# Performance work log

Measured on AMD Instinct MI355X. Metric: run time of the kernel, lower is better.

## Reference

```python
import jax, jax.numpy as jnp
import numpy as np
import math
from functools import partial

SIGMA0 = 12.0
KSIZE = int(2 * (4.0 * SIGMA0 + 0.5))  # 97, already odd
if KSIZE % 2 == 0:
    KSIZE -= 1


def _gauss1d(ksize, sigma):
    # kornia-style gaussian; ksize is odd so no half-pixel shift
    x = jnp.arange(ksize, dtype=jnp.float32) - ksize // 2
    g = jnp.exp(-(x ** 2) / (2.0 * sigma ** 2))
    return g / g.sum()


def _blur(x, sigma):
    # x: (N,1,H,W). filter2d with outer(kx,ky) kernel and constant(zero) border
    # == two separable 1D convs with zero 'SAME' padding.
    k = _gauss1d(KSIZE, sigma)
    dn = ('NCHW', 'OIHW', 'NCHW')
    x = jax.lax.conv_general_dilated(x, k[None, None, :, None], (1, 1), 'SAME', dimension_numbers=dn)
    x = jax.lax.conv_general_dilated(x, k[None, None, None, :], (1, 1), 'SAME', dimension_numbers=dn)
    return x


def _grid_sample_bilinear(img, grid):
    # img: (N,C,H,W); grid: (N,H,W,2) with last dim (x,y) in [-1,1], align_corners=True
    N, C, H, W = img.shape
    x = (grid[..., 0] + 1.0) * 0.5 * (W - 1)
    y = (grid[..., 1] + 1.0) * 0.5 * (H - 1)
    x0 = jnp.floor(x); y0 = jnp.floor(y)
    wx = x - x0; wy = y - y0
    x0i = jnp.clip(x0, 0, W - 1).astype(jnp.int32)
    x1i = jnp.clip(x0 + 1, 0, W - 1).astype(jnp.int32)
    y0i = jnp.clip(y0, 0, H - 1).astype(jnp.int32)
    y1i = jnp.clip(y0 + 1, 0, H - 1).astype(jnp.int32)
    flat = img.reshape(N, C, H * W)

    def gather(yi, xi):
        idx = (yi * W + xi).reshape(N, 1, H * W)
        return jnp.take_along_axis(flat, idx, axis=2).reshape(N, C, H, W)

    wx = wx[:, None]; wy = wy[:, None]  # broadcast over C
    top = gather(y0i, x0i) * (1 - wx) + gather(y0i, x1i) * wx
    bot = gather(y1i, x0i) * (1 - wx) + gather(y1i, x1i) * wx
    return top * (1 - wy) + bot * wy


def _elastic(t, d_rand, sigma, alpha):
    # t: (1,C,H,W); d_rand: (1,2,H,W) uniform [0,1]
    n, c, h, w = t.shape
    d = d_rand * 2.0 - 1.0
    dy = _blur(d[:, 0:1], sigma[0]) * alpha[0]   # (1,1,H,W)
    dx = _blur(d[:, 1:2], sigma[1]) * alpha[1]
    d_yx = jnp.concatenate([dy, dx], axis=1).transpose(0, 2, 3, 1)  # (1,H,W,2) = (dy,dx)
    xs = jnp.linspace(-1.0, 1.0, w, dtype=t.dtype)
    ys = jnp.linspace(-1.0, 1.0, h, dtype=t.dtype)
    gx, gy = jnp.meshgrid(xs, ys)  # (H,W)
    grid = jnp.stack([gx, gy], axis=-1)[None]  # (1,H,W,2) (x,y)
    # NOTE: faithful to source: dy is added to x-coord, dx to y-coord
    return _grid_sample_bilinear(t, jnp.clip(grid + d_yx, -1.0, 1.0))


def setup_inputs() -> dict:
    key = jax.random.key(0)
    k1, k2, k3 = jax.random.split(key, 3)
    H = W = 2048
    return {
        'image': jax.random.normal(k1, (3, H, W), dtype=jnp.float32),
        'mask': (jax.random.uniform(k2, (1, H, W)) > 0.5).astype(jnp.float32),
        'd_rand': jax.random.uniform(k3, (1, 2, H, W), dtype=jnp.float32),
        'log_sigma': jnp.full((2,), math.log(12.0), dtype=jnp.float32),
        'log_alpha': jnp.zeros((2,), dtype=jnp.float32),
    }


def reference(image, mask, d_rand, log_sigma, log_alpha):
    sigma = jnp.exp(log_sigma)
    alpha = jnp.exp(log_alpha)
    img_out = _elastic(image[None], d_rand, sigma, alpha)[0]
    msk_out = _elastic(mask[None], d_rand, sigma, alpha)[0]
    return (img_out, msk_out)
```

## Files before the change

### kernel.cpp

```cpp
#include <hip/hip_runtime.h>

#define H 2048
#define W 2048
#define KS 97
#define KH 48
#define KPAD 112
#define TR 16
#define RING 24
#define NB 1024

typedef float  nfloat4 __attribute__((ext_vector_type(4)));
typedef _Float16 h4v   __attribute__((ext_vector_type(4)));
typedef _Float16 h8v   __attribute__((ext_vector_type(8)));

__global__ __launch_bounds__(128) void make_weights_k(const float* __restrict__ log_sigma,
                                                      const float* __restrict__ log_alpha,
                                                      float* __restrict__ wts) {
    __shared__ float e0s[KS], e1s[KS];
    __shared__ float sums[2];
    const int t = threadIdx.x;
    const float s0 = expf(log_sigma[0]);
    const float s1 = expf(log_sigma[1]);
    if (t < KS) {
        const float xx = (float)(t - KH);
        e0s[t] = expf(-(xx * xx) / (2.f * s0 * s0));
        e1s[t] = expf(-(xx * xx) / (2.f * s1 * s1));
    }
    __syncthreads();
    if (t == 0) {
        float a = 0.f, b = 0.f;
        for (int k = 0; k < KS; ++k) { a += e0s[k]; b += e1s[k]; }
        sums[0] = a; sums[1] = b;
    }
    __syncthreads();
    if (t < KPAD) {
        wts[t]        = (t < KS) ? e0s[t] / sums[0] : 0.f;
        wts[KPAD + t] = (t < KS) ? e1s[t] / sums[1] : 0.f;
    }
    if (t == 0) {
        wts[2 * KPAD]     = expf(log_alpha[0]);
        wts[2 * KPAD + 1] = expf(log_alpha[1]);
    }
}

__device__ __forceinline__ void vblur_body_fast(const float* __restrict__ src,
                                                const float* __restrict__ g,
                                                float* __restrict__ dst,
                                                int col, int i0) {
    const float* __restrict__ p = src + (size_t)(i0 - KH) * W + col;
    float2 win[RING];
    float2 acc[TR];
#pragma unroll
    for (int t = 0; t < TR; ++t) acc[t] = make_float2(0.f, 0.f);
#pragma unroll
    for (int j = 0; j < RING; ++j) win[j] = *(const float2*)(p + (size_t)j * W);

    const float* __restrict__ q = p + (size_t)RING * W;

    for (int m = 0; m < 3; ++m) {
#pragma unroll
        for (int r = 0; r < 24; ++r) {
            const float2 nv = *(const float2*)(q + (size_t)r * W);
            const float gk = g[m * 24 + r];
#pragma unroll
            for (int t = 0; t < TR; ++t) {
                const int w = (r + t) < 24 ? (r + t) : (r + t - 24);
                acc[t].x = fmaf(gk, win[w].x, acc[t].x);
                acc[t].y = fmaf(gk, win[w].y, acc[t].y);
            }
            win[r] = nv;
        }
        q += (size_t)24 * W;
    }
    {
#pragma unroll
        for (int r = 0; r < 24; ++r) {
            float2 nv;
            if (r <= 15)
                nv = *(const float2*)(q + (size_t)r * W);
            const float gk = g[72 + r];
#pragma unroll
            for (int t = 0; t < TR; ++t) {
                const int w = (r + t) < 24 ? (r + t) : (r + t - 24);
                acc[t].x = fmaf(gk, win[w].x, acc[t].x);
                acc[t].y = fmaf(gk, win[w].y, acc[t].y);
            }
            if (r <= 15)
                win[r] = nv;
        }
    }
    {
        const float gk = g[96];
#pragma unroll
        for (int t = 0; t < TR; ++t) {
            acc[t].x = fmaf(gk, win[t].x, acc[t].x);
            acc[t].y = fmaf(gk, win[t].y, acc[t].y);
        }
    }
#pragma unroll
    for (int t = 0; t < TR; ++t)
        *(float2*)(dst + (size_t)(i0 + t) * W + col) = acc[t];
}

__device__ __forceinline__ float2 vload_row_g(const float* __restrict__ src, int row, int col) {
    float2 v = make_float2(0.5f, 0.5f);
    if ((unsigned)row < (unsigned)H)
        v = *(const float2*)(src + (size_t)row * W + col);
    return v;
}

__device__ __forceinline__ void vblur_body_guard(const float* __restrict__ src,
                                                 const float* __restrict__ g,
                                                 float* __restrict__ dst,
                                                 int col, int i0) {
    const int base = i0 - KH;
    float2 win[RING];
    float2 acc[TR];
#pragma unroll
    for (int t = 0; t < TR; ++t) acc[t] = make_float2(0.f, 0.f);
#pragma unroll
    for (int j = 0; j < RING; ++j) win[j] = vload_row_g(src, base + j, col);

    for (int m = 0; m < 3; ++m) {
        const int kb = m * 24;
#pragma unroll
        for (int r = 0; r < 24; ++r) {
            const float gk = g[kb + r];
#pragma unroll
            for (int t = 0; t < TR; ++t) {
                const int w = (r + t) < 24 ? (r + t) : (r + t - 24);
                acc[t].x = fmaf(gk, win[w].x, acc[t].x);
                acc[t].y = fmaf(gk, win[w].y, acc[t].y);
            }
            win[r] = vload_row_g(src, base + kb + r + 24, col);
        }
    }
    {
#pragma unroll
        for (int r = 0; r < 24; ++r) {
            const float gk = g[72 + r];
#pragma unroll
            for (int t = 0; t < TR; ++t) {
                const int w = (r + t) < 24 ? (r + t) : (r + t - 24);
                acc[t].x = fmaf(gk, win[w].x, acc[t].x);
                acc[t].y = fmaf(gk, win[w].y, acc[t].y);
            }
            if (r <= 15)
                win[r] = vload_row_g(src, base + 96 + r, col);
        }
    }
    {
        const float gk = g[96];
#pragma unroll
        for (int t = 0; t < TR; ++t) {
            acc[t].x = fmaf(gk, win[t].x, acc[t].x);
            acc[t].y = fmaf(gk, win[t].y, acc[t].y);
        }
    }
#pragma unroll
    for (int t = 0; t < TR; ++t)
        *(float2*)(dst + (size_t)(i0 + t) * W + col) = acc[t];
}

__global__ __launch_bounds__(512, 4) void pv_k(const float* __restrict__ drand,
                                               const float* __restrict__ wts,
                                               const float* __restrict__ image,
                                               const float* __restrict__ mask,
                                               float* __restrict__ tmp,
                                               h4v* __restrict__ packed) {
    const size_t HW = (size_t)H * W;
    const int bid = blockIdx.x;
    const int tid = threadIdx.x;
    if (tid < 256) {
        const int c   = bid >> 9;
        const int id  = bid & 511;
        const int xcd = id & 7;
        const int seq = id >> 3;
        const int yb  = xcd * 16 + (seq >> 2);
        const int xb  = seq & 3;
        const int col = (xb * 256 + tid) * 2;
        const int i0  = yb * TR;
        const float* __restrict__ src = drand + (size_t)c * HW;
        const float* __restrict__ g   = wts + c * KPAD;
        float* __restrict__ dst       = tmp + (size_t)c * HW;
        if (i0 >= KH && i0 + 63 <= H - 1)
            vblur_body_fast(src, g, dst, col, i0);
        else
            vblur_body_guard(src, g, dst, col, i0);
    } else if (packed) {
        const int lt = tid - 256;
#pragma unroll
        for (int it = 0; it < 4; ++it) {
            const size_t idx4 = ((size_t)bid * 1024 + it * 256 + lt) * 4;
            const float4 p0 = *(const float4*)(image + idx4);
            const float4 p1 = *(const float4*)(image + HW + idx4);
            const float4 p2 = *(const float4*)(image + 2 * HW + idx4);
            const float4 pm = *(const float4*)(mask + idx4);
            h8v lo, hi;
            lo[0] = (_Float16)p0.x; lo[1] = (_Float16)p1.x; lo[2] = (_Float16)p2.x; lo[3] = (_Float16)pm.x;
            lo[4] = (_Float16)p0.y; lo[5] = (_Float16)p1.y; lo[6] = (_Float16)p2.y; lo[7] = (_Float16)pm.y;
            hi[0] = (_Float16)p0.z; hi[1] = (_Float16)p1.z; hi[2] = (_Float16)p2.z; hi[3] = (_Float16)pm.z;
            hi[4] = (_Float16)p0.w; hi[5] = (_Float16)p1.w; hi[6] = (_Float16)p2.w; hi[7] = (_Float16)pm.w;
            *(h8v*)(packed + idx4)     = lo;
            *(h8v*)(packed + idx4 + 2) = hi;
        }
    }
}

#define SW 2160
template <bool PACKED>
__global__ __launch_bounds__(512) void hblur_sample_k(const float* __restrict__ tmp,
                                                      const float* __restrict__ wts,
                                                      const float* __restrict__ image,
                                                      const float* __restrict__ mask,
                                                      const h4v* __restrict__ packed,
                                                      float* __restrict__ out) {
    const int i   = (blockIdx.x & 7) * 256 + (blockIdx.x >> 3);
    const int tid = threadIdx.x;

    __shared__ __align__(16) float s0[SW];
    __shared__ __align__(16) float s1[SW];
    __shared__ __align__(16) float g0s[KPAD];
    __shared__ __align__(16) float g1s[KPAD];

    if (tid < KPAD) { g0s[tid] = wts[tid]; g1s[tid] = wts[KPAD + tid]; }

    const float* __restrict__ t0 = tmp + (size_t)i * W;
    const float* __restrict__ t1 = tmp + (size_t)H * W + (size_t)i * W;
    for (int idx = tid; idx < SW / 4; idx += 512) {
        const int colb = idx * 4 - KH;
        float4 v0 = make_float4(0.5f, 0.5f, 0.5f, 0.5f);
        float4 v1 = v0;
        if (colb >= 0 && colb + 3 < W) {
            v0 = *(const float4*)(t0 + colb);
            v1 = *(const float4*)(t1 + colb);
        }
        *(float4*)(s0 + idx * 4) = v0;
        *(float4*)(s1 + idx * 4) = v1;
    }
    __syncthreads();

    const int lb = tid * 4;

    float4 A0 = *(const float4*)(s0 + lb), B0 = *(const float4*)(s0 + lb + 4);
    float4 A1 = *(const float4*)(s1 + lb), B1 = *(const float4*)(s1 + lb + 4);
    float dy[4] = {0.f, 0.f, 0.f, 0.f}, dx[4] = {0.f, 0.f, 0.f, 0.f};

#pragma unroll
    for (int kg = 0; kg < 26; ++kg) {
        const int k0 = kg * 4;
        const float4 g0q = *(const float4*)(g0s + k0);
        const float4 g1q = *(const float4*)(g1s + k0);
        const float4 N0  = *(const float4*)(s0 + lb + k0 + 8);
        const float4 N1  = *(const float4*)(s1 + lb + k0 + 8);
        const float e0[8] = {A0.x, A0.y, A0.z, A0.w, B0.x, B0.y, B0.z, B0.w};
        const float e1[8] = {A1.x, A1.y, A1.z, A1.w, B1.x, B1.y, B1.z, B1.w};
#pragma unroll
        for (int j = 0; j < 4; ++j) {
            const float gj0 = j == 0 ? g0q.x : j == 1 ? g0q.y : j == 2 ? g0q.z : g0q.w;
            const float gj1 = j == 0 ? g1q.x : j == 1 ? g1q.y : j == 2 ? g1q.z : g1q.w;
#pragma unroll
            for (int c = 0; c < 4; ++c) {
                dy[c] = fmaf(gj0, e0[c + j], dy[c]);
                dx[c] = fmaf(gj1, e1[c + j], dx[c]);
            }
        }
        A0 = B0; B0 = N0; A1 = B1; B1 = N1;
    }

    const float a0 = wts[2 * KPAD];
    const float a1 = wts[2 * KPAD + 1];
    const float a0x2 = a0 + a0;
    const float a1x2 = a1 + a1;
    const float step = 2.f / 2047.f;
    float res[4][4];
#pragma unroll
    for (int c = 0; c < 4; ++c) {
        const int j = lb + c;
        const float dyc = fmaf(dy[c], a0x2, -a0);
        const float dxc = fmaf(dx[c], a1x2, -a1);
        float xn = -1.f + (float)j * step + dyc;
        float yn = -1.f + (float)i * step + dxc;
        xn = fminf(fmaxf(xn, -1.f), 1.f);
        yn = fminf(fmaxf(yn, -1.f), 1.f);

        const float x = (xn + 1.f) * 0.5f * (float)(W - 1);
        const float y = (yn + 1.f) * 0.5f * (float)(H - 1);
        const float x0f = floorf(x), y0f = floorf(y);
        const float wx = x - x0f, wy = y - y0f;

        int x0 = (int)x0f, y0 = (int)y0f;
        int x1 = x0 + 1, y1 = y0 + 1;
        x0 = min(max(x0, 0), W - 1); x1 = min(max(x1, 0), W - 1);
        y0 = min(max(y0, 0), H - 1); y1 = min(max(y1, 0), H - 1);

        const float w00 = (1.f - wx) * (1.f - wy);
        const float w10 = wx * (1.f - wy);
        const float w01 = (1.f - wx) * wy;
        const float w11 = wx * wy;

        const size_t i00 = (size_t)y0 * W + x0;
        const size_t i10 = (size_t)y0 * W + x1;
        const size_t i01 = (size_t)y1 * W + x0;
        const size_t i11 = (size_t)y1 * W + x1;

        if (PACKED) {
            const h4v v00 = packed[i00], v10 = packed[i10];
            const h4v v01 = packed[i01], v11 = packed[i11];
            res[0][c] = (float)v00[0] * w00 + (float)v10[0] * w10 + (float)v01[0] * w01 + (float)v11[0] * w11;
            res[1][c] = (float)v00[1] * w00 + (float)v10[1] * w10 + (float)v01[1] * w01 + (float)v11[1] * w11;
            res[2][c] = (float)v00[2] * w00 + (float)v10[2] * w10 + (float)v01[2] * w01 + (float)v11[2] * w11;
            res[3][c] = (float)v00[3] * w00 + (float)v10[3] * w10 + (float)v01[3] * w01 + (float)v11[3] * w11;
        } else {
#pragma unroll
            for (int p = 0; p < 3; ++p) {
                const float* __restrict__ pl = image + (size_t)p * H * W;
                res[p][c] = pl[i00] * w00 + pl[i10] * w10 + pl[i01] * w01 + pl[i11] * w11;
            }
            res[3][c] = mask[i00] * w00 + mask[i10] * w10 + mask[i01] * w01 + mask[i11] * w11;
        }
    }

    const size_t o = (size_t)i * W + lb;
#pragma unroll
    for (int p = 0; p < 4; ++p) {
        nfloat4 v;
        v.x = res[p][0]; v.y = res[p][1]; v.z = res[p][2]; v.w = res[p][3];
        __builtin_nontemporal_store(v, (nfloat4*)(out + (size_t)p * H * W + o));
    }
}

extern "C" void kernel_launch(void* const* d_in, const int* in_sizes, int n_in,
                              void* d_out, int out_size, void* d_ws, size_t ws_size,
                              hipStream_t stream) {
    const float* image     = (const float*)d_in[0];
    const float* mask      = (const float*)d_in[1];
    const float* drand     = (const float*)d_in[2];
    const float* log_sigma = (const float*)d_in[3];
    const float* log_alpha = (const float*)d_in[4];
    float* out = (float*)d_out;

    const size_t HW = (size_t)H * W;
    const bool can_pack = ws_size >= HW * 8 + 2 * HW * 4 + 1024;

    h4v* packed; float* tmp; float* wts;
    if (can_pack) {
        packed = (h4v*)d_ws;
        tmp    = (float*)((char*)d_ws + HW * 8);
        wts    = tmp + 2 * HW;
    } else {
        packed = nullptr;
        tmp    = (float*)d_ws;
        wts    = tmp + 2 * HW;
    }

    make_weights_k<<<1, 128, 0, stream>>>(log_sigma, log_alpha, wts);
    pv_k<<<NB, 512, 0, stream>>>(drand, wts, image, mask, tmp, packed);
    if (can_pack)
        hblur_sample_k<true><<<H, 512, 0, stream>>>(tmp, wts, image, mask, packed, out);
    else
        hblur_sample_k<false><<<H, 512, 0, stream>>>(tmp, wts, image, mask, packed, out);
}
```

Before: 240.4 us.

## Split vertical-blur and packing into separate 256-thread blocks with smaller row tiles

Shrinks the vertical-blur output tile from 16 to 8 rows per thread and its sliding window from 24 to 16 rows, so ring indexing becomes a power-of-two mask. Blocks drop from 512 to 256 threads, and the image/mask fp16 packing moves out of the upper half of each blur block into its own blocks, interleaved one blur block to two pack blocks. The aim is lower register pressure, higher occupancy and better load balance between the compute-heavy blur and the bandwidth-bound packing. In exchange, each output row costs more re-read input rows, since there are 97+7 loads for 8 outputs instead of 97+15 for 16.

```diff
diff --git a/kernel.cpp b/kernel.cpp
--- a/kernel.cpp
+++ b/kernel.cpp
@@ -5,9 +5,10 @@
 #define KS 97
 #define KH 48
 #define KPAD 112
-#define TR 16
-#define RING 24
-#define NB 1024
+#define TR 8
+#define NB_VB 2048
+#define NB_PK 4096
+#define NB_TOT (NB_VB + NB_PK)
 
 typedef float  nfloat4 __attribute__((ext_vector_type(4)));
 typedef _Float16 h4v   __attribute__((ext_vector_type(4)));
@@ -48,44 +49,44 @@
                                                 float* __restrict__ dst,
                                                 int col, int i0) {
     const float* __restrict__ p = src + (size_t)(i0 - KH) * W + col;
-    float2 win[RING];
+    float2 win[16];
     float2 acc[TR];
 #pragma unroll
     for (int t = 0; t < TR; ++t) acc[t] = make_float2(0.f, 0.f);
 #pragma unroll
-    for (int j = 0; j < RING; ++j) win[j] = *(const float2*)(p + (size_t)j * W);
-
-    const float* __restrict__ q = p + (size_t)RING * W;
-
-    for (int m = 0; m < 3; ++m) {
-#pragma unroll
-        for (int r = 0; r < 24; ++r) {
+    for (int j = 0; j < 16; ++j) win[j] = *(const float2*)(p + (size_t)j * W);
+
+    const float* __restrict__ q = p + (size_t)16 * W;
+
+    for (int m = 0; m < 5; ++m) {
+#pragma unroll
+        for (int r = 0; r < 16; ++r) {
             const float2 nv = *(const float2*)(q + (size_t)r * W);
-            const float gk = g[m * 24 + r];
+            const float gk = g[m * 16 + r];
 #pragma unroll
             for (int t = 0; t < TR; ++t) {
-                const int w = (r + t) < 24 ? (r + t) : (r + t - 24);
-                acc[t].x = fmaf(gk, win[w].x, acc[t].x);
-                acc[t].y = fmaf(gk, win[w].y, acc[t].y);
+                const float2 u = win[(r + t) & 15];
+                acc[t].x = fmaf(gk, u.x, acc[t].x);
+                acc[t].y = fmaf(gk, u.y, acc[t].y);
             }
             win[r] = nv;
         }
-        q += (size_t)24 * W;
+        q += (size_t)16 * W;
     }
     {
 #pragma unroll
-        for (int r = 0; r < 24; ++r) {
+        for (int r = 0; r < 16; ++r) {
             float2 nv;
-            if (r <= 15)
+            if (r <= 7)
                 nv = *(const float2*)(q + (size_t)r * W);
-            const float gk = g[72 + r];
+            const float gk = g[80 + r];
 #pragma unroll
             for (int t = 0; t < TR; ++t) {
-                const int w = (r + t) < 24 ? (r + t) : (r + t - 24);
-                acc[t].x = fmaf(gk, win[w].x, acc[t].x);
-                acc[t].y = fmaf(gk, win[w].y, acc[t].y);
-            }
-            if (r <= 15)
+                const float2 u = win[(r + t) & 15];
+                acc[t].x = fmaf(gk, u.x, acc[t].x);
+                acc[t].y = fmaf(gk, u.y, acc[t].y);
+            }
+            if (r <= 7)
                 win[r] = nv;
         }
     }
@@ -114,38 +115,38 @@
                                                  float* __restrict__ dst,
                                                  int col, int i0) {
     const int base = i0 - KH;
-    float2 win[RING];
+    float2 win[16];
     float2 acc[TR];
 #pragma unroll
     for (int t = 0; t < TR; ++t) acc[t] = make_float2(0.f, 0.f);
 #pragma unroll
-    for (int j = 0; j < RING; ++j) win[j] = vload_row_g(src, base + j, col);
-
-    for (int m = 0; m < 3; ++m) {
-        const int kb = m * 24;
-#pragma unroll
-        for (int r = 0; r < 24; ++r) {
+    for (int j = 0; j < 16; ++j) win[j] = vload_row_g(src, base + j, col);
+
+    for (int m = 0; m < 5; ++m) {
+        const int kb = m * 16;
+#pragma unroll
+        for (int r = 0; r < 16; ++r) {
             const float gk = g[kb + r];
 #pragma unroll
             for (int t = 0; t < TR; ++t) {
-                const int w = (r + t) < 24 ? (r + t) : (r + t - 24);
-                acc[t].x = fmaf(gk, win[w].x, acc[t].x);
-                acc[t].y = fmaf(gk, win[w].y, acc[t].y);
-            }
-            win[r] = vload_row_g(src, base + kb + r + 24, col);
+                const float2 u = win[(r + t) & 15];
+                acc[t].x = fmaf(gk, u.x, acc[t].x);
+                acc[t].y = fmaf(gk, u.y, acc[t].y);
+            }
+            win[r] = vload_row_g(src, base + kb + r + 16, col);
         }
     }
     {
 #pragma unroll
-        for (int r = 0; r < 24; ++r) {
-            const float gk = g[72 + r];
+        for (int r = 0; r < 16; ++r) {
+            const float gk = g[80 + r];
 #pragma unroll
             for (int t = 0; t < TR; ++t) {
-                const int w = (r + t) < 24 ? (r + t) : (r + t - 24);
-                acc[t].x = fmaf(gk, win[w].x, acc[t].x);
-                acc[t].y = fmaf(gk, win[w].y, acc[t].y);
-            }
-            if (r <= 15)
+                const float2 u = win[(r + t) & 15];
+                acc[t].x = fmaf(gk, u.x, acc[t].x);
+                acc[t].y = fmaf(gk, u.y, acc[t].y);
+            }
+            if (r <= 7)
                 win[r] = vload_row_g(src, base + 96 + r, col);
         }
     }
@@ -162,7 +163,7 @@
         *(float2*)(dst + (size_t)(i0 + t) * W + col) = acc[t];
 }
 
-__global__ __launch_bounds__(512, 4) void pv_k(const float* __restrict__ drand,
+__global__ __launch_bounds__(256, 8) void pv_k(const float* __restrict__ drand,
                                                const float* __restrict__ wts,
                                                const float* __restrict__ image,
                                                const float* __restrict__ mask,
@@ -171,39 +172,38 @@
     const size_t HW = (size_t)H * W;
     const int bid = blockIdx.x;
     const int tid = threadIdx.x;
-    if (tid < 256) {
-        const int c   = bid >> 9;
-        const int id  = bid & 511;
+    const bool do_vb = (bid % 3 == 0) || !packed;
+    if (do_vb) {
+        const int vb  = packed ? (bid / 3) : bid;
+        const int c   = vb >> 10;
+        const int id  = vb & 1023;
         const int xcd = id & 7;
         const int seq = id >> 3;
-        const int yb  = xcd * 16 + (seq >> 2);
+        const int strip = xcd * 32 + (seq >> 2);
         const int xb  = seq & 3;
         const int col = (xb * 256 + tid) * 2;
-        const int i0  = yb * TR;
+        const int i0  = strip * TR;
         const float* __restrict__ src = drand + (size_t)c * HW;
         const float* __restrict__ g   = wts + c * KPAD;
         float* __restrict__ dst       = tmp + (size_t)c * HW;
-        if (i0 >= KH && i0 + 63 <= H - 1)
+        if (i0 >= KH && i0 + 55 <= H - 1)
             vblur_body_fast(src, g, dst, col, i0);
         else
             vblur_body_guard(src, g, dst, col, i0);
-    } else if (packed) {
-        const int lt = tid - 256;
-#pragma unroll
-        for (int it = 0; it < 4; ++it) {
-            const size_t idx4 = ((size_t)bid * 1024 + it * 256 + lt) * 4;
-            const float4 p0 = *(const float4*)(image + idx4);
-            const float4 p1 = *(const float4*)(image + HW + idx4);
-            const float4 p2 = *(const float4*)(image + 2 * HW + idx4);
-            const float4 pm = *(const float4*)(mask + idx4);
-            h8v lo, hi;
-            lo[0] = (_Float16)p0.x; lo[1] = (_Float16)p1.x; lo[2] = (_Float16)p2.x; lo[3] = (_Float16)pm.x;
-            lo[4] = (_Float16)p0.y; lo[5] = (_Float16)p1.y; lo[6] = (_Float16)p2.y; lo[7] = (_Float16)pm.y;
-            hi[0] = (_Float16)p0.z; hi[1] = (_Float16)p1.z; hi[2] = (_Float16)p2.z; hi[3] = (_Float16)pm.z;
-            hi[4] = (_Float16)p0.w; hi[5] = (_Float16)p1.w; hi[6] = (_Float16)p2.w; hi[7] = (_Float16)pm.w;
-            *(h8v*)(packed + idx4)     = lo;
-            *(h8v*)(packed + idx4 + 2) = hi;
-        }
+    } else {
+        const int pk = bid - bid / 3 - 1;
+        const size_t idx4 = ((size_t)pk * 256 + tid) * 4;
+        const float4 p0 = *(const float4*)(image + idx4);
+        const float4 p1 = *(const float4*)(image + HW + idx4);
+        const float4 p2 = *(const float4*)(image + 2 * HW + idx4);
+        const float4 pm = *(const float4*)(mask + idx4);
+        h8v lo, hi;
+        lo[0] = (_Float16)p0.x; lo[1] = (_Float16)p1.x; lo[2] = (_Float16)p2.x; lo[3] = (_Float16)pm.x;
+        lo[4] = (_Float16)p0.y; lo[5] = (_Float16)p1.y; lo[6] = (_Float16)p2.y; lo[7] = (_Float16)pm.y;
+        hi[0] = (_Float16)p0.z; hi[1] = (_Float16)p1.z; hi[2] = (_Float16)p2.z; hi[3] = (_Float16)pm.z;
+        hi[4] = (_Float16)p0.w; hi[5] = (_Float16)p1.w; hi[6] = (_Float16)p2.w; hi[7] = (_Float16)pm.w;
+        *(h8v*)(packed + idx4)     = lo;
+        *(h8v*)(packed + idx4 + 2) = hi;
     }
 }
 
@@ -355,7 +355,8 @@
     }
 
     make_weights_k<<<1, 128, 0, stream>>>(log_sigma, log_alpha, wts);
-    pv_k<<<NB, 512, 0, stream>>>(drand, wts, image, mask, tmp, packed);
+    pv_k<<<can_pack ? NB_TOT : NB_VB, 256, 0, stream>>>(drand, wts, image, mask,
+                                                        tmp, packed);
     if (can_pack)
         hblur_sample_k<true><<<H, 512, 0, stream>>>(tmp, wts, image, mask, packed, out);
     else
```

Result: slower. 318.1 us (+32.3%).
